# Performance work log

Hardware: AMD Instinct MI355X
Metric: run time of the kernel (lower is better)

## Reference

```python
import jax, jax.numpy as jnp
import numpy as np

# hyperparameters from init_kwargs
TEMP = 0.05
MOMENTUM = 0.2
ALPHA = 0.9
TEMP_DIST = 0.6
LAMBDA1 = 1.0
LAMBDA2 = 1.0
EPS_CONS = 2.0
NUM_SAMPLES = 8192
NUM_FEATURES = 2048
B = 256
K = 20
EPS = 1e-12


def setup_inputs() -> dict:
    key = jax.random.key(0)
    ks = jax.random.split(key, 8)
    inputs0 = jax.random.normal(ks[0], (B, NUM_FEATURES), dtype=jnp.float32)
    logits0 = jax.random.normal(ks[1], (B, NUM_SAMPLES), dtype=jnp.float32)
    logits1 = jax.random.normal(ks[2], (B, NUM_SAMPLES), dtype=jnp.float32)
    targets = jax.random.randint(ks[3], (B,), 0, NUM_SAMPLES, dtype=jnp.int32)
    indexes = jnp.arange(B, dtype=jnp.int32)  # global idx == batch idx (identity idx2bidx)
    neighbors = jax.random.randint(ks[4], (B, K), 0, B, dtype=jnp.int32)
    neighbor_dists = jax.random.uniform(ks[5], (B, K), dtype=jnp.float32)
    rampup = jnp.ones((), dtype=jnp.float32)
    features = jax.random.normal(ks[6], (NUM_SAMPLES, NUM_FEATURES), dtype=jnp.float32)
    features = features / jnp.linalg.norm(features, axis=1, keepdims=True)
    return {
        'inputs0': inputs0, 'logits0': logits0, 'logits1': logits1,
        'targets': targets, 'indexes': indexes, 'neighbors': neighbors,
        'neighbor_dists': neighbor_dists, 'rampup': rampup, 'features': features,
    }


def reference(inputs0, logits0, logits1, targets, indexes, neighbors,
              neighbor_dists, rampup, features):
    # F.normalize(inputs[0], dim=1)
    x = inputs0 / jnp.maximum(jnp.linalg.norm(inputs0, axis=1, keepdims=True), EPS)

    # CM forward: scores against memory bank, scaled by temperature
    outputs = (x @ features.T) / TEMP                      # [B, S]
    logp = jax.nn.log_softmax(outputs, axis=-1)
    loss_nce = -jnp.mean(jnp.take_along_axis(logp, targets[:, None], axis=1))

    targets_onehot = jax.nn.one_hot(targets, NUM_SAMPLES, dtype=logits0.dtype)

    # neighbor gathering: indexes = arange(B) so idx2bidx is identity; every
    # neighbor in [0,B) passes the `nb in indexes` filter.
    p0 = jax.nn.softmax(logits0, axis=-1)[neighbors]       # [B, K, S]
    p1 = jax.nn.softmax(logits1, axis=-1)[neighbors]       # [B, K, S]
    # loop appends logits0-row then logits1-row per neighbor -> interleave
    p = jnp.stack([p0, p1], axis=2).reshape(B, 2 * K, NUM_SAMPLES)
    d2 = jnp.repeat(neighbor_dists, 2, axis=1)             # [B, 2K] (d,d pairs)
    w = jax.nn.softmax(d2 / TEMP_DIST, axis=1)             # [B, 2K]
    logits_neighbors1 = jnp.einsum('bk,bks->bs', w, p)     # [B, S]

    # KL branch: neighbors with dist <= eps_consistency (all, since eps=2.0)
    mask = (neighbor_dists <= EPS_CONS).astype(p0.dtype)   # [B, K]
    cnt = jnp.maximum(mask.sum(axis=1, keepdims=True), 1.0)
    logits_neighbors1_KL = jnp.einsum('bk,bks->bs', mask, p0) / cnt  # [B, S]

    refined = ALPHA * targets_onehot + (1.0 - ALPHA) * jax.lax.stop_gradient(logits_neighbors1)
    loss_ce = jnp.mean(jnp.sum(-refined * jax.nn.log_softmax(logits0, axis=-1), axis=1))

    # KLDivLoss(logsoftmax(logits1).detach(), target) with batchmean reduction
    lp1 = jax.lax.stop_gradient(jax.nn.log_softmax(logits1, axis=-1))
    t = logits_neighbors1_KL
    kl = jnp.sum(jnp.where(t > 0, t * (jnp.log(jnp.maximum(t, EPS)) - lp1), 0.0)) / B

    # CM momentum memory-bank scatter update (backward side-effect in torch);
    # equivalent to the sequential loop when targets are unique in the batch.
    upd = MOMENTUM * features[targets] + (1.0 - MOMENTUM) * x
    upd = upd / jnp.maximum(jnp.linalg.norm(upd, axis=1, keepdims=True), EPS)
    new_features = features.at[targets].set(upd)

    return (loss_nce, LAMBDA1 * loss_ce, LAMBDA2 * rampup * kl, new_features)
```

## Files before the change

### kernel.cpp

```cpp
#include <hip/hip_runtime.h>
#include <cmath>

#define NB 256
#define NS 8192
#define NF 2048
#define NK 20

typedef _Float16 half8 __attribute__((ext_vector_type(8)));
typedef _Float16 half4 __attribute__((ext_vector_type(4)));
typedef float f32x4 __attribute__((ext_vector_type(4)));

__device__ __forceinline__ void async16(const void* g, void* l) {
  __builtin_amdgcn_global_load_lds(
      (const __attribute__((address_space(1))) unsigned int*)g,
      (__attribute__((address_space(3))) unsigned int*)l, 16, 0, 0);
}

__device__ __forceinline__ float waveSum(float v) {
#pragma unroll
  for (int off = 32; off > 0; off >>= 1) v += __shfl_xor(v, off, 64);
  return v;
}
__device__ __forceinline__ float waveMax(float v) {
#pragma unroll
  for (int off = 32; off > 0; off >>= 1) v = fmaxf(v, __shfl_xor(v, off, 64));
  return v;
}

__global__ __launch_bounds__(256, 1) void prep(
    const float* __restrict__ in0, const float* __restrict__ logits0,
    const float* __restrict__ logits1, const int* __restrict__ neighbors,
    const float* __restrict__ ndist, _Float16* __restrict__ Pt,
    _Float16* __restrict__ xh, _Float16* __restrict__ alpha_h,
    float* __restrict__ mll, _Float16* __restrict__ Wp,
    float* __restrict__ loss) {
  __shared__ alignas(16) union {
    struct {
      float redA[4];
      float redB[4];
    } s;
    _Float16 Lt[16 * 520];
  } sm;
  int tid = threadIdx.x, blk = blockIdx.x;
  int wave = tid >> 6, lane = tid & 63;

  if (blk < 512) {
    int r = blk;
    const float* src = (r < NB) ? logits0 : logits1;
    const float4* row = (const float4*)(src + (size_t)(r & (NB - 1)) * NS);
    float4 v[8];
    float mx = -1e30f;
#pragma unroll
    for (int i = 0; i < 8; ++i) {
      v[i] = row[tid + i * 256];
      mx = fmaxf(mx, fmaxf(fmaxf(v[i].x, v[i].y), fmaxf(v[i].z, v[i].w)));
    }
    float wv = waveMax(mx);
    if (lane == 0) sm.s.redA[wave] = wv;
    __syncthreads();
    float m = fmaxf(fmaxf(sm.s.redA[0], sm.s.redA[1]), fmaxf(sm.s.redA[2], sm.s.redA[3]));
    float se = 0.0f;
#pragma unroll
    for (int i = 0; i < 8; ++i)
      se += expf(v[i].x - m) + expf(v[i].y - m) + expf(v[i].z - m) + expf(v[i].w - m);
    float sw = waveSum(se);
    if (lane == 0) sm.s.redB[wave] = sw;
    __syncthreads();
    float l = (sm.s.redB[0] + sm.s.redB[1]) + (sm.s.redB[2] + sm.s.redB[3]);
    if (tid == 0) {
      mll[r] = m + logf(l);
      alpha_h[r] = (_Float16)(256.0f * expf(-m) / l);
    }
  } else if (blk < 1024) {
    int s0 = (blk - 512) * 16;
#pragma unroll
    for (int g = 0; g < 8; ++g) {
      int pos = g * 256 + tid;
      int row = pos >> 2, c4 = pos & 3;
      const float* src = ((row < NB) ? logits0 + (size_t)row * NS
                                     : logits1 + (size_t)(row - NB) * NS) + s0 + c4 * 4;
      float4 v = *(const float4*)src;
      sm.Lt[(c4 * 4 + 0) * 520 + row] = (_Float16)expf(v.x);
      sm.Lt[(c4 * 4 + 1) * 520 + row] = (_Float16)expf(v.y);
      sm.Lt[(c4 * 4 + 2) * 520 + row] = (_Float16)expf(v.z);
      sm.Lt[(c4 * 4 + 3) * 520 + row] = (_Float16)expf(v.w);
    }
    __syncthreads();
    int srow = tid >> 4, seg = tid & 15;
    _Float16* dst = Pt + (size_t)(s0 + srow) * 512 + seg * 32;
    const _Float16* lsrc = &sm.Lt[srow * 520 + seg * 32];
#pragma unroll
    for (int q = 0; q < 4; ++q)
      *(half8*)(dst + q * 8) = *(const half8*)(lsrc + q * 8);
  } else if (blk < 1280) {
    int b = blk - 1024;
    const float4* row = (const float4*)(in0 + (size_t)b * NF);
    float4 v0 = row[tid], v1 = row[tid + 256];
    float ss = v0.x * v0.x + v0.y * v0.y + v0.z * v0.z + v0.w * v0.w +
               v1.x * v1.x + v1.y * v1.y + v1.z * v1.z + v1.w * v1.w;
    float w = waveSum(ss);
    if (lane == 0) sm.s.redA[wave] = w;
    __syncthreads();
    float tot = (sm.s.redA[0] + sm.s.redA[1]) + (sm.s.redA[2] + sm.s.redA[3]);
    float inv = 1.0f / fmaxf(sqrtf(tot), 1e-12f);
    half4 h0, h1;
    h0[0] = (_Float16)(v0.x * inv); h0[1] = (_Float16)(v0.y * inv);
    h0[2] = (_Float16)(v0.z * inv); h0[3] = (_Float16)(v0.w * inv);
    h1[0] = (_Float16)(v1.x * inv); h1[1] = (_Float16)(v1.y * inv);
    h1[2] = (_Float16)(v1.z * inv); h1[3] = (_Float16)(v1.w * inv);
    ((half4*)(xh + (size_t)b * NF))[tid] = h0;
    ((half4*)(xh + (size_t)b * NF))[tid + 256] = h1;
  } else {
    if (tid < 3) loss[tid] = 0.0f;
    float4* W4 = (float4*)Wp;
    for (int i = tid; i < 512 * 512 * 2 / 16; i += 256) W4[i] = make_float4(0, 0, 0, 0);
    __syncthreads();
    int b = tid;
    float d[NK], e[NK];
    int n[NK];
    float s = 0.0f;
    int cnt = 0;
#pragma unroll
    for (int k = 0; k < NK; ++k) {
      d[k] = ndist[b * NK + k];
      n[k] = neighbors[b * NK + k];
      e[k] = expf(d[k] * (1.0f / 0.6f));
      s += e[k];
      cnt += (d[k] <= 2.0f) ? 1 : 0;
    }
    float invs = 1.0f / (2.0f * s);
    float invc = 1.0f / fmaxf((float)cnt, 1.0f);
    _Float16* rkl = Wp + (size_t)b * 512;
    _Float16* rce = Wp + (size_t)(256 + b) * 512;
#pragma unroll
    for (int k = 0; k < NK; ++k) {
      bool first = true;
#pragma unroll
      for (int k2 = 0; k2 < NK; ++k2)
        if (k2 < k && n[k2] == n[k]) first = false;
      if (first) {
        float wsum = 0.0f, ksum = 0.0f;
#pragma unroll
        for (int k2 = 0; k2 < NK; ++k2)
          if (k2 >= k && n[k2] == n[k]) {
            wsum += e[k2] * invs;
            ksum += (d[k2] <= 2.0f) ? invc : 0.0f;
          }
        rkl[n[k]] = (_Float16)ksum;
        rce[n[k]] = (_Float16)wsum;
        rce[256 + n[k]] = (_Float16)wsum;
      }
    }
  }
}

__global__ __launch_bounds__(256) void gemms(
    const _Float16* __restrict__ xh, const float* __restrict__ fB,
    const _Float16* __restrict__ Wp, const _Float16* __restrict__ Pt,
    const _Float16* __restrict__ alpha_h,
    const float* __restrict__ logits0, const float* __restrict__ logits1,
    const float* __restrict__ mll, const int* __restrict__ targets,
    float* __restrict__ outF, float* __restrict__ pm, float* __restrict__ pl,
    float* __restrict__ tgt, float* __restrict__ part) {
  __shared__ alignas(16) _Float16 As[128 * 64];
  __shared__ alignas(16) _Float16 Bs[128 * 64];
  __shared__ alignas(16) _Float16 Al[512];
  __shared__ float red[4];
  int tid = threadIdx.x, wave = tid >> 6, lane = tid & 63;
  int quad = lane >> 4, r16 = lane & 15, lrow = lane >> 3, lch = lane & 7;
  int blk = blockIdx.x;
  if (blk < 256) {
    int bx = blk & 127, by = blk >> 7;
    int n0 = bx * 64, m0 = by * 128;
    int c4 = tid & 15, rbase = tid >> 4;
    f32x4 acc[2][4] = {};
    for (int k0 = 0; k0 < NF; k0 += 64) {
      float4 bv[4];
#pragma unroll
      for (int ss = 0; ss < 4; ++ss)
        bv[ss] = *(const float4*)(fB + (size_t)(n0 + ss * 16 + rbase) * NF + k0 + c4 * 4);
      __syncthreads();
#pragma unroll
      for (int ss = 0; ss < 4; ++ss) {
        int rl = ss * 32 + wave * 8 + lrow;
        int sc = lch ^ (rl & 7);
        async16(xh + (size_t)(m0 + rl) * NF + k0 + sc * 8, &As[rl * 64 + lch * 8]);
      }
#pragma unroll
      for (int ss = 0; ss < 4; ++ss) {
        int row = ss * 16 + rbase;
        half4 h;
        h[0] = (_Float16)bv[ss].x; h[1] = (_Float16)bv[ss].y;
        h[2] = (_Float16)bv[ss].z; h[3] = (_Float16)bv[ss].w;
        int pc = (((c4 >> 1) ^ (row & 7)) << 3) + ((c4 & 1) << 2);
        *(half4*)&Bs[row * 64 + pc] = h;
        if (by == 0)
          *(float4*)(outF + (size_t)(n0 + row) * NF + k0 + c4 * 4) = bv[ss];
      }
      __syncthreads();
#pragma unroll
      for (int sub = 0; sub < 2; ++sub) {
        int slot = ((sub * 4 + quad) ^ (r16 & 7)) * 8;
        half8 af[2], bf[4];
#pragma unroll
        for (int i = 0; i < 2; ++i)
          af[i] = *(const half8*)&As[(wave * 32 + i * 16 + r16) * 64 + slot];
#pragma unroll
        for (int j = 0; j < 4; ++j)
          bf[j] = *(const half8*)&Bs[(j * 16 + r16) * 64 + slot];
#pragma unroll
        for (int i = 0; i < 2; ++i)
#pragma unroll
          for (int j = 0; j < 4; ++j)
            acc[i][j] = __builtin_amdgcn_mfma_f32_16x16x32_f16(af[i], bf[j], acc[i][j], 0, 0, 0);
      }
    }
#pragma unroll
    for (int i = 0; i < 2; ++i)
#pragma unroll
      for (int r = 0; r < 4; ++r) {
        int R = m0 + wave * 32 + i * 16 + quad * 4 + r;
        float sv[4];
#pragma unroll
        for (int j = 0; j < 4; ++j) sv[j] = acc[i][j][r] * 20.0f;
        float mx = fmaxf(fmaxf(sv[0], sv[1]), fmaxf(sv[2], sv[3]));
#pragma unroll
        for (int m2 = 1; m2 < 16; m2 <<= 1) mx = fmaxf(mx, __shfl_xor(mx, m2, 64));
        float e = expf(sv[0] - mx) + expf(sv[1] - mx) + expf(sv[2] - mx) + expf(sv[3] - mx);
#pragma unroll
        for (int m2 = 1; m2 < 16; m2 <<= 1) e += __shfl_xor(e, m2, 64);
        int tg = targets[R];
#pragma unroll
        for (int j = 0; j < 4; ++j)
          if (n0 + j * 16 + r16 == tg) tgt[R] = sv[j];
        if (r16 == 0) { pm[R * 128 + bx] = mx; pl[R * 128 + bx] = e; }
      }
  } else {
    int nb = blk - 256;
    int bx = nb & 63, by = nb >> 6;
    int n0 = bx * 128, m0 = by * 128;
    int wm = (wave >> 1) * 64, wn = (wave & 1) * 64;
    if (tid < 64) ((half8*)Al)[tid] = ((const half8*)alpha_h)[tid];
    f32x4 acc[4][4] = {};
    for (int k0 = 0; k0 < 512; k0 += 64) {
      __syncthreads();
#pragma unroll
      for (int ss = 0; ss < 4; ++ss) {
        int rl = ss * 32 + wave * 8 + lrow;
        int sc = lch ^ (rl & 7);
        async16(Wp + (size_t)(m0 + rl) * 512 + k0 + sc * 8, &As[rl * 64 + lch * 8]);
        async16(Pt + (size_t)(n0 + rl) * 512 + k0 + sc * 8, &Bs[rl * 64 + lch * 8]);
      }
      __syncthreads();
#pragma unroll
      for (int sub = 0; sub < 2; ++sub) {
        int slot = ((sub * 4 + quad) ^ (r16 & 7)) * 8;
        half8 alv = *(const half8*)&Al[k0 + slot];
        half8 af[4], bf[4];
#pragma unroll
        for (int i = 0; i < 4; ++i)
          af[i] = *(const half8*)&As[(wm + i * 16 + r16) * 64 + slot];
#pragma unroll
        for (int j = 0; j < 4; ++j)
          bf[j] = *(const half8*)&Bs[(wn + j * 16 + r16) * 64 + slot] * alv;
#pragma unroll
        for (int i = 0; i < 4; ++i)
#pragma unroll
          for (int j = 0; j < 4; ++j)
            acc[i][j] = __builtin_amdgcn_mfma_f32_16x16x32_f16(af[i], bf[j], acc[i][j], 0, 0, 0);
      }
    }
    bool iskl = (by < 2);
    const float* lgbase = iskl ? logits1 : logits0;
    float local = 0.0f;
#pragma unroll
    for (int i = 0; i < 4; ++i)
#pragma unroll
      for (int r = 0; r < 4; ++r) {
        int Mg = m0 + wm + i * 16 + quad * 4 + r;
        int b = iskl ? Mg : (Mg - 256);
        float mv = mll[iskl ? 256 + b : b];
        const float* lgrow = lgbase + (size_t)b * NS + n0 + wn;
#pragma unroll
        for (int j = 0; j < 4; ++j) {
          float lg = lgrow[j * 16 + r16];
          float t = acc[i][j][r] * (1.0f / 256.0f);
          if (iskl)
            local += (t > 0.0f) ? t * (logf(fmaxf(t, 1e-12f)) - (lg - mv)) : 0.0f;
          else
            local += -0.1f * t * (lg - mv);
        }
      }
    float wsv = waveSum(local);
    if (lane == 0) red[wave] = wsv;
    __syncthreads();
    if (tid == 0) part[nb] = (red[0] + red[1]) + (red[2] + red[3]);
  }
}

__global__ __launch_bounds__(128) void final_reduce(
    const float* __restrict__ pm, const float* __restrict__ pl,
    const float* __restrict__ tgt, const float* __restrict__ part,
    const float* __restrict__ logits0, const float* __restrict__ mll,
    const int* __restrict__ targets, const float* __restrict__ rampup,
    const float* __restrict__ in0, const float* __restrict__ features,
    float* __restrict__ outF, float* __restrict__ out) {
  __shared__ float rA[2], rB[2];
  __shared__ int flag;
  int tid = threadIdx.x, blk = blockIdx.x;
  if (blk < 256) {
    int b = blk;
    float m = pm[b * 128 + tid];
    float l = pl[b * 128 + tid];
    float wm = waveMax(m);
    if ((tid & 63) == 0) rA[tid >> 6] = wm;
    __syncthreads();
    float mx = fmaxf(rA[0], rA[1]);
    float e = l * expf(m - mx);
    float ws = waveSum(e);
    if ((tid & 63) == 0) rB[tid >> 6] = ws;
    __syncthreads();
    if (tid == 0) {
      float S = rB[0] + rB[1];
      float nce = -(tgt[b] - mx - logf(S));
      int tg = targets[b];
      float oh = -0.9f * (logits0[(size_t)b * NS + tg] - mll[b]);
      float pb = part[b];
      float v1 = oh;
      if (b >= 128) v1 += pb;
      atomicAdd(out + 0, nce * (1.0f / 256.0f));
      atomicAdd(out + 1, v1 * (1.0f / 256.0f));
      if (b < 128) atomicAdd(out + 2, rampup[0] * pb * (1.0f / 256.0f));
    }
  } else {
    int b = blk - 256;
    int tg = targets[b];
    if (tid == 0) flag = 0;
    __syncthreads();
    bool later = false;
    for (int i = b + 1 + tid; i < 256; i += 128) later = later || (targets[i] == tg);
    if (later) flag = 1;
    __syncthreads();
    if (flag) return;
    const float4* xr = (const float4*)(in0 + (size_t)b * NF);
    const float4* fr = (const float4*)(features + (size_t)tg * NF);
    float4 a[4];
    float ssx = 0.0f;
#pragma unroll
    for (int s = 0; s < 4; ++s) {
      a[s] = xr[tid + s * 128];
      ssx += a[s].x * a[s].x + a[s].y * a[s].y + a[s].z * a[s].z + a[s].w * a[s].w;
    }
    float w1 = waveSum(ssx);
    if ((tid & 63) == 0) rA[tid >> 6] = w1;
    __syncthreads();
    float ix = 0.8f / fmaxf(sqrtf(rA[0] + rA[1]), 1e-12f);
    float4 v[4];
    float ss = 0.0f;
#pragma unroll
    for (int s = 0; s < 4; ++s) {
      float4 f = fr[tid + s * 128];
      v[s] = make_float4(0.2f * f.x + ix * a[s].x, 0.2f * f.y + ix * a[s].y,
                         0.2f * f.z + ix * a[s].z, 0.2f * f.w + ix * a[s].w);
      ss += v[s].x * v[s].x + v[s].y * v[s].y + v[s].z * v[s].z + v[s].w * v[s].w;
    }
    float w2 = waveSum(ss);
    if ((tid & 63) == 0) rB[tid >> 6] = w2;
    __syncthreads();
    float inv = 1.0f / fmaxf(sqrtf(rB[0] + rB[1]), 1e-12f);
    float4* o4 = (float4*)(outF + (size_t)tg * NF);
#pragma unroll
    for (int s = 0; s < 4; ++s)
      o4[tid + s * 128] = make_float4(v[s].x * inv, v[s].y * inv, v[s].z * inv, v[s].w * inv);
  }
}

extern "C" void kernel_launch(void* const* d_in, const int* in_sizes, int n_in,
                              void* d_out, int out_size, void* d_ws, size_t ws_size,
                              hipStream_t stream) {
  const float* inputs0 = (const float*)d_in[0];
  const float* logits0 = (const float*)d_in[1];
  const float* logits1 = (const float*)d_in[2];
  const int* targets = (const int*)d_in[3];
  const int* neighbors = (const int*)d_in[5];
  const float* ndist = (const float*)d_in[6];
  const float* rampup = (const float*)d_in[7];
  const float* features = (const float*)d_in[8];
  float* out = (float*)d_out;

  char* ws = (char*)d_ws;
  float* mll = (float*)(ws + 4096);
  _Float16* alpha_h = (_Float16*)(ws + 8192);
  float* part = (float*)(ws + 12288);
  float* tgt = (float*)(ws + 16384);
  float* pm = (float*)(ws + 65536);
  float* pl = (float*)(ws + 196608);
  _Float16* Wp = (_Float16*)(ws + 524288);
  _Float16* xh = (_Float16*)(ws + (3 << 20));
  _Float16* Pt = (_Float16*)(ws + (4 << 20));

  prep<<<1281, 256, 0, stream>>>(inputs0, logits0, logits1, neighbors, ndist,
                                 Pt, xh, alpha_h, mll, Wp, out);
  gemms<<<512, 256, 0, stream>>>(xh, features, Wp, Pt, alpha_h, logits0, logits1,
                                 mll, targets, out + 3, pm, pl, tgt, part);
  final_reduce<<<512, 128, 0, stream>>>(pm, pl, tgt, part, logits0, mll, targets,
                                        rampup, inputs0, features, out + 3, out);
}
```

Before: 209.9 us.

## Parallelize neighbor-weight prep across blocks and deepen GEMM K-tile

The single prep block that zeroed the whole weight matrix and built every row's neighbor weights is split into 256 blocks. Each block zeroes its own two rows and builds them with one thread, which removes a long serial tail from the prep kernel. The first GEMM stage now uses a K-tile of 128 instead of 64, halving the number of loop iterations and barriers, at the cost of more LDS. The fp32 feature copy to the output is now split between the two row-tile blocks, half of the K range each, instead of being done only by the first block.

```diff
diff --git a/kernel.cpp b/kernel.cpp
--- a/kernel.cpp
+++ b/kernel.cpp
@@ -45,6 +45,7 @@
   int wave = tid >> 6, lane = tid & 63;
 
   if (blk < 512) {
+    if (blk == 0 && tid < 3) loss[tid] = 0.0f;
     int r = blk;
     const float* src = (r < NB) ? logits0 : logits1;
     const float4* row = (const float4*)(src + (size_t)(r & (NB - 1)) * NS);
@@ -111,44 +112,45 @@
     ((half4*)(xh + (size_t)b * NF))[tid] = h0;
     ((half4*)(xh + (size_t)b * NF))[tid + 256] = h1;
   } else {
-    if (tid < 3) loss[tid] = 0.0f;
-    float4* W4 = (float4*)Wp;
-    for (int i = tid; i < 512 * 512 * 2 / 16; i += 256) W4[i] = make_float4(0, 0, 0, 0);
-    __syncthreads();
-    int b = tid;
-    float d[NK], e[NK];
-    int n[NK];
-    float s = 0.0f;
-    int cnt = 0;
-#pragma unroll
-    for (int k = 0; k < NK; ++k) {
-      d[k] = ndist[b * NK + k];
-      n[k] = neighbors[b * NK + k];
-      e[k] = expf(d[k] * (1.0f / 0.6f));
-      s += e[k];
-      cnt += (d[k] <= 2.0f) ? 1 : 0;
-    }
-    float invs = 1.0f / (2.0f * s);
-    float invc = 1.0f / fmaxf((float)cnt, 1.0f);
+    int b = blk - 1280;
     _Float16* rkl = Wp + (size_t)b * 512;
     _Float16* rce = Wp + (size_t)(256 + b) * 512;
-#pragma unroll
-    for (int k = 0; k < NK; ++k) {
-      bool first = true;
-#pragma unroll
-      for (int k2 = 0; k2 < NK; ++k2)
-        if (k2 < k && n[k2] == n[k]) first = false;
-      if (first) {
-        float wsum = 0.0f, ksum = 0.0f;
+    if (tid < 64) ((float4*)rkl)[tid] = make_float4(0, 0, 0, 0);
+    else if (tid < 128) ((float4*)rce)[tid - 64] = make_float4(0, 0, 0, 0);
+    __syncthreads();
+    if (tid == 0) {
+      float d[NK], e[NK];
+      int n[NK];
+      float s = 0.0f;
+      int cnt = 0;
+#pragma unroll
+      for (int k = 0; k < NK; ++k) {
+        d[k] = ndist[b * NK + k];
+        n[k] = neighbors[b * NK + k];
+        e[k] = expf(d[k] * (1.0f / 0.6f));
+        s += e[k];
+        cnt += (d[k] <= 2.0f) ? 1 : 0;
+      }
+      float invs = 1.0f / (2.0f * s);
+      float invc = 1.0f / fmaxf((float)cnt, 1.0f);
+#pragma unroll
+      for (int k = 0; k < NK; ++k) {
+        bool first = true;
 #pragma unroll
         for (int k2 = 0; k2 < NK; ++k2)
-          if (k2 >= k && n[k2] == n[k]) {
-            wsum += e[k2] * invs;
-            ksum += (d[k2] <= 2.0f) ? invc : 0.0f;
-          }
-        rkl[n[k]] = (_Float16)ksum;
-        rce[n[k]] = (_Float16)wsum;
-        rce[256 + n[k]] = (_Float16)wsum;
+          if (k2 < k && n[k2] == n[k]) first = false;
+        if (first) {
+          float wsum = 0.0f, ksum = 0.0f;
+#pragma unroll
+          for (int k2 = 0; k2 < NK; ++k2)
+            if (k2 >= k && n[k2] == n[k]) {
+              wsum += e[k2] * invs;
+              ksum += (d[k2] <= 2.0f) ? invc : 0.0f;
+            }
+          rkl[n[k]] = (_Float16)ksum;
+          rce[n[k]] = (_Float16)wsum;
+          rce[256 + n[k]] = (_Float16)wsum;
+        }
       }
     }
   }
@@ -162,7 +164,7 @@
     const float* __restrict__ mll, const int* __restrict__ targets,
     float* __restrict__ outF, float* __restrict__ pm, float* __restrict__ pl,
     float* __restrict__ tgt, float* __restrict__ part) {
-  __shared__ alignas(16) _Float16 As[128 * 64];
+  __shared__ alignas(16) _Float16 As[128 * 128];
   __shared__ alignas(16) _Float16 Bs[128 * 64];
   __shared__ alignas(16) _Float16 Al[512];
   __shared__ float red[4];
@@ -172,42 +174,53 @@
   if (blk < 256) {
     int bx = blk & 127, by = blk >> 7;
     int n0 = bx * 64, m0 = by * 128;
-    int c4 = tid & 15, rbase = tid >> 4;
+    int rr = tid >> 4, cc = tid & 15;
     f32x4 acc[2][4] = {};
-    for (int k0 = 0; k0 < NF; k0 += 64) {
-      float4 bv[4];
-#pragma unroll
-      for (int ss = 0; ss < 4; ++ss)
-        bv[ss] = *(const float4*)(fB + (size_t)(n0 + ss * 16 + rbase) * NF + k0 + c4 * 4);
+    for (int k0 = 0; k0 < NF; k0 += 128) {
       __syncthreads();
+      float4 bv[4][2];
 #pragma unroll
       for (int ss = 0; ss < 4; ++ss) {
-        int rl = ss * 32 + wave * 8 + lrow;
-        int sc = lch ^ (rl & 7);
-        async16(xh + (size_t)(m0 + rl) * NF + k0 + sc * 8, &As[rl * 64 + lch * 8]);
-      }
+        int row = ss * 16 + rr;
+        int sc = cc ^ (row & 7);
+        const float* src = fB + (size_t)(n0 + row) * NF + k0 + sc * 8;
+        bv[ss][0] = *(const float4*)src;
+        bv[ss][1] = *(const float4*)(src + 4);
+      }
+#pragma unroll
+      for (int ss = 0; ss < 8; ++ss) {
+        int row = ss * 16 + rr;
+        int sc = cc ^ (row & 7);
+        async16(xh + (size_t)(m0 + row) * NF + k0 + sc * 8, &As[row * 128 + cc * 8]);
+      }
+      bool doStore = (by == ((k0 >= NF / 2) ? 1 : 0));
 #pragma unroll
       for (int ss = 0; ss < 4; ++ss) {
-        int row = ss * 16 + rbase;
-        half4 h;
-        h[0] = (_Float16)bv[ss].x; h[1] = (_Float16)bv[ss].y;
-        h[2] = (_Float16)bv[ss].z; h[3] = (_Float16)bv[ss].w;
-        int pc = (((c4 >> 1) ^ (row & 7)) << 3) + ((c4 & 1) << 2);
-        *(half4*)&Bs[row * 64 + pc] = h;
-        if (by == 0)
-          *(float4*)(outF + (size_t)(n0 + row) * NF + k0 + c4 * 4) = bv[ss];
+        int row = ss * 16 + rr;
+        int sc = cc ^ (row & 7);
+        half8 h;
+        h[0] = (_Float16)bv[ss][0].x; h[1] = (_Float16)bv[ss][0].y;
+        h[2] = (_Float16)bv[ss][0].z; h[3] = (_Float16)bv[ss][0].w;
+        h[4] = (_Float16)bv[ss][1].x; h[5] = (_Float16)bv[ss][1].y;
+        h[6] = (_Float16)bv[ss][1].z; h[7] = (_Float16)bv[ss][1].w;
+        *(half8*)&Bs[row * 128 + cc * 8] = h;
+        if (doStore) {
+          float4* o = (float4*)(outF + (size_t)(n0 + row) * NF + k0 + sc * 8);
+          o[0] = bv[ss][0];
+          o[1] = bv[ss][1];
+        }
       }
       __syncthreads();
 #pragma unroll
-      for (int sub = 0; sub < 2; ++sub) {
+      for (int sub = 0; sub < 4; ++sub) {
         int slot = ((sub * 4 + quad) ^ (r16 & 7)) * 8;
         half8 af[2], bf[4];
 #pragma unroll
         for (int i = 0; i < 2; ++i)
-          af[i] = *(const half8*)&As[(wave * 32 + i * 16 + r16) * 64 + slot];
+          af[i] = *(const half8*)&As[(wave * 32 + i * 16 + r16) * 128 + slot];
 #pragma unroll
         for (int j = 0; j < 4; ++j)
-          bf[j] = *(const half8*)&Bs[(j * 16 + r16) * 64 + slot];
+          bf[j] = *(const half8*)&Bs[(j * 16 + r16) * 128 + slot];
 #pragma unroll
         for (int i = 0; i < 2; ++i)
 #pragma unroll
@@ -399,7 +412,7 @@
   _Float16* xh = (_Float16*)(ws + (3 << 20));
   _Float16* Pt = (_Float16*)(ws + (4 << 20));
 
-  prep<<<1281, 256, 0, stream>>>(inputs0, logits0, logits1, neighbors, ndist,
+  prep<<<1536, 256, 0, stream>>>(inputs0, logits0, logits1, neighbors, ndist,
                                  Pt, xh, alpha_h, mll, Wp, out);
   gemms<<<512, 256, 0, stream>>>(xh, features, Wp, Pt, alpha_h, logits0, logits1,
                                  mll, targets, out + 3, pm, pl, tgt, part);
```

Result: faster. 195.7 us (-6.8%).

## Replace neighbor-weight GEMM with direct gather-accumulate and widen feature GEMM tiles

Applied to the files above, without the earlier changes.

Drops the dense weight-matrix GEMM that mixed neighbor probabilities through a transposed exp table. Each block now gathers the 20 neighbor rows of a row-major fp16 exp table directly and accumulates the CE and KL targets, writing the loss terms with atomics. This also removes the zeroing and building of the weight matrix. The feature GEMM now uses 256x64 tiles so each features column-block is read and copied once instead of twice. The cost is uncoalesced-ish gathered reads and a larger LDS footprint per block.

```diff
diff --git a/kernel.cpp b/kernel.cpp
--- a/kernel.cpp
+++ b/kernel.cpp
@@ -27,24 +27,17 @@
   return v;
 }
 
-__global__ __launch_bounds__(256, 1) void prep(
+__global__ __launch_bounds__(256) void prep(
     const float* __restrict__ in0, const float* __restrict__ logits0,
-    const float* __restrict__ logits1, const int* __restrict__ neighbors,
-    const float* __restrict__ ndist, _Float16* __restrict__ Pt,
-    _Float16* __restrict__ xh, _Float16* __restrict__ alpha_h,
-    float* __restrict__ mll, _Float16* __restrict__ Wp,
-    float* __restrict__ loss) {
-  __shared__ alignas(16) union {
-    struct {
-      float redA[4];
-      float redB[4];
-    } s;
-    _Float16 Lt[16 * 520];
-  } sm;
+    const float* __restrict__ logits1, _Float16* __restrict__ P,
+    _Float16* __restrict__ xh, float* __restrict__ alpha,
+    float* __restrict__ mll, float* __restrict__ loss) {
+  __shared__ float redA[4], redB[4];
   int tid = threadIdx.x, blk = blockIdx.x;
   int wave = tid >> 6, lane = tid & 63;
 
   if (blk < 512) {
+    if (blk == 0 && tid < 3) loss[tid] = 0.0f;
     int r = blk;
     const float* src = (r < NB) ? logits0 : logits1;
     const float4* row = (const float4*)(src + (size_t)(r & (NB - 1)) * NS);
@@ -56,52 +49,40 @@
       mx = fmaxf(mx, fmaxf(fmaxf(v[i].x, v[i].y), fmaxf(v[i].z, v[i].w)));
     }
     float wv = waveMax(mx);
-    if (lane == 0) sm.s.redA[wave] = wv;
-    __syncthreads();
-    float m = fmaxf(fmaxf(sm.s.redA[0], sm.s.redA[1]), fmaxf(sm.s.redA[2], sm.s.redA[3]));
+    if (lane == 0) redA[wave] = wv;
+    __syncthreads();
+    float m = fmaxf(fmaxf(redA[0], redA[1]), fmaxf(redA[2], redA[3]));
+    float em = expf(m);
     float se = 0.0f;
-#pragma unroll
-    for (int i = 0; i < 8; ++i)
-      se += expf(v[i].x - m) + expf(v[i].y - m) + expf(v[i].z - m) + expf(v[i].w - m);
+    half4* prow = (half4*)(P + (size_t)r * NS);
+#pragma unroll
+    for (int i = 0; i < 8; ++i) {
+      float e0 = expf(v[i].x - m), e1 = expf(v[i].y - m);
+      float e2 = expf(v[i].z - m), e3 = expf(v[i].w - m);
+      se += (e0 + e1) + (e2 + e3);
+      half4 h;
+      h[0] = (_Float16)(e0 * em); h[1] = (_Float16)(e1 * em);
+      h[2] = (_Float16)(e2 * em); h[3] = (_Float16)(e3 * em);
+      prow[tid + i * 256] = h;
+    }
     float sw = waveSum(se);
-    if (lane == 0) sm.s.redB[wave] = sw;
-    __syncthreads();
-    float l = (sm.s.redB[0] + sm.s.redB[1]) + (sm.s.redB[2] + sm.s.redB[3]);
+    if (lane == 0) redB[wave] = sw;
+    __syncthreads();
+    float l = (redB[0] + redB[1]) + (redB[2] + redB[3]);
     if (tid == 0) {
       mll[r] = m + logf(l);
-      alpha_h[r] = (_Float16)(256.0f * expf(-m) / l);
-    }
-  } else if (blk < 1024) {
-    int s0 = (blk - 512) * 16;
-#pragma unroll
-    for (int g = 0; g < 8; ++g) {
-      int pos = g * 256 + tid;
-      int row = pos >> 2, c4 = pos & 3;
-      const float* src = ((row < NB) ? logits0 + (size_t)row * NS
-                                     : logits1 + (size_t)(row - NB) * NS) + s0 + c4 * 4;
-      float4 v = *(const float4*)src;
-      sm.Lt[(c4 * 4 + 0) * 520 + row] = (_Float16)expf(v.x);
-      sm.Lt[(c4 * 4 + 1) * 520 + row] = (_Float16)expf(v.y);
-      sm.Lt[(c4 * 4 + 2) * 520 + row] = (_Float16)expf(v.z);
-      sm.Lt[(c4 * 4 + 3) * 520 + row] = (_Float16)expf(v.w);
-    }
-    __syncthreads();
-    int srow = tid >> 4, seg = tid & 15;
-    _Float16* dst = Pt + (size_t)(s0 + srow) * 512 + seg * 32;
-    const _Float16* lsrc = &sm.Lt[srow * 520 + seg * 32];
-#pragma unroll
-    for (int q = 0; q < 4; ++q)
-      *(half8*)(dst + q * 8) = *(const half8*)(lsrc + q * 8);
-  } else if (blk < 1280) {
-    int b = blk - 1024;
+      alpha[r] = 256.0f * expf(-m) / l;
+    }
+  } else {
+    int b = blk - 512;
     const float4* row = (const float4*)(in0 + (size_t)b * NF);
     float4 v0 = row[tid], v1 = row[tid + 256];
     float ss = v0.x * v0.x + v0.y * v0.y + v0.z * v0.z + v0.w * v0.w +
                v1.x * v1.x + v1.y * v1.y + v1.z * v1.z + v1.w * v1.w;
     float w = waveSum(ss);
-    if (lane == 0) sm.s.redA[wave] = w;
-    __syncthreads();
-    float tot = (sm.s.redA[0] + sm.s.redA[1]) + (sm.s.redA[2] + sm.s.redA[3]);
+    if (lane == 0) redA[wave] = w;
+    __syncthreads();
+    float tot = (redA[0] + redA[1]) + (redA[2] + redA[3]);
     float inv = 1.0f / fmaxf(sqrtf(tot), 1e-12f);
     half4 h0, h1;
     h0[0] = (_Float16)(v0.x * inv); h0[1] = (_Float16)(v0.y * inv);
@@ -110,199 +91,156 @@
     h1[2] = (_Float16)(v1.z * inv); h1[3] = (_Float16)(v1.w * inv);
     ((half4*)(xh + (size_t)b * NF))[tid] = h0;
     ((half4*)(xh + (size_t)b * NF))[tid + 256] = h1;
+  }
+}
+
+__global__ __launch_bounds__(256) void fused2(
+    const _Float16* __restrict__ xh, const float* __restrict__ fB,
+    const _Float16* __restrict__ P, const float* __restrict__ alpha,
+    const float* __restrict__ mll, const float* __restrict__ logits0,
+    const float* __restrict__ logits1, const int* __restrict__ targets,
+    const int* __restrict__ neighbors, const float* __restrict__ ndist,
+    const float* __restrict__ rampup, float* __restrict__ outF,
+    float* __restrict__ pm, float* __restrict__ pl, float* __restrict__ tgt,
+    float* __restrict__ out) {
+  __shared__ alignas(16) _Float16 As[256 * 64];
+  __shared__ alignas(16) _Float16 Bs[64 * 64];
+  __shared__ float red[8];
+  int tid = threadIdx.x, wave = tid >> 6, lane = tid & 63;
+  int quad = lane >> 4, r16 = lane & 15;
+  int blk = blockIdx.x;
+
+  if (blk < 128) {
+    int n0 = blk * 64;
+    int srow = tid >> 2, scg = tid & 3;
+    f32x4 acc[4][4] = {};
+    for (int k0 = 0; k0 < NF; k0 += 64) {
+      float4 fv[4];
+      const float* bsrc = fB + (size_t)(n0 + srow) * NF + k0 + scg * 16;
+#pragma unroll
+      for (int q = 0; q < 4; ++q) fv[q] = *(const float4*)(bsrc + q * 4);
+      __syncthreads();
+#pragma unroll
+      for (int ss = 0; ss < 8; ++ss) {
+        int rl = ss * 32 + (tid >> 3);
+        int sc = (tid & 7) ^ (rl & 7);
+        async16(xh + (size_t)rl * NF + k0 + sc * 8, &As[rl * 64 + (tid & 7) * 8]);
+      }
+#pragma unroll
+      for (int h = 0; h < 2; ++h) {
+        half8 hh;
+        hh[0] = (_Float16)fv[2 * h].x; hh[1] = (_Float16)fv[2 * h].y;
+        hh[2] = (_Float16)fv[2 * h].z; hh[3] = (_Float16)fv[2 * h].w;
+        hh[4] = (_Float16)fv[2 * h + 1].x; hh[5] = (_Float16)fv[2 * h + 1].y;
+        hh[6] = (_Float16)fv[2 * h + 1].z; hh[7] = (_Float16)fv[2 * h + 1].w;
+        int p = (scg * 2 + h) ^ (srow & 7);
+        *(half8*)&Bs[srow * 64 + p * 8] = hh;
+      }
+      float4* odst = (float4*)(outF + (size_t)(n0 + srow) * NF + k0 + scg * 16);
+#pragma unroll
+      for (int q = 0; q < 4; ++q) odst[q] = fv[q];
+      __syncthreads();
+#pragma unroll
+      for (int sub = 0; sub < 2; ++sub) {
+        int slot = ((sub * 4 + quad) ^ (r16 & 7)) * 8;
+        half8 af[4], bf[4];
+#pragma unroll
+        for (int i = 0; i < 4; ++i)
+          af[i] = *(const half8*)&As[(wave * 64 + i * 16 + r16) * 64 + slot];
+#pragma unroll
+        for (int j = 0; j < 4; ++j)
+          bf[j] = *(const half8*)&Bs[(j * 16 + r16) * 64 + slot];
+#pragma unroll
+        for (int i = 0; i < 4; ++i)
+#pragma unroll
+          for (int j = 0; j < 4; ++j)
+            acc[i][j] = __builtin_amdgcn_mfma_f32_16x16x32_f16(af[i], bf[j], acc[i][j], 0, 0, 0);
+      }
+    }
+#pragma unroll
+    for (int i = 0; i < 4; ++i)
+#pragma unroll
+      for (int r = 0; r < 4; ++r) {
+        int R = wave * 64 + i * 16 + quad * 4 + r;
+        float sv[4];
+#pragma unroll
+        for (int j = 0; j < 4; ++j) sv[j] = acc[i][j][r] * 20.0f;
+        float mx = fmaxf(fmaxf(sv[0], sv[1]), fmaxf(sv[2], sv[3]));
+#pragma unroll
+        for (int m2 = 1; m2 < 16; m2 <<= 1) mx = fmaxf(mx, __shfl_xor(mx, m2, 64));
+        float e = expf(sv[0] - mx) + expf(sv[1] - mx) + expf(sv[2] - mx) + expf(sv[3] - mx);
+#pragma unroll
+        for (int m2 = 1; m2 < 16; m2 <<= 1) e += __shfl_xor(e, m2, 64);
+        int tg = targets[R];
+#pragma unroll
+        for (int j = 0; j < 4; ++j)
+          if (n0 + j * 16 + r16 == tg) tgt[R] = sv[j];
+        if (r16 == 0) { pm[R * 128 + blk] = mx; pl[R * 128 + blk] = e; }
+      }
   } else {
-    if (tid < 3) loss[tid] = 0.0f;
-    float4* W4 = (float4*)Wp;
-    for (int i = tid; i < 512 * 512 * 2 / 16; i += 256) W4[i] = make_float4(0, 0, 0, 0);
-    __syncthreads();
-    int b = tid;
-    float d[NK], e[NK];
-    int n[NK];
+    int gb = blk - 128;
+    int b = gb >> 2, s0 = (gb & 3) * 2048;
     float s = 0.0f;
     int cnt = 0;
 #pragma unroll
     for (int k = 0; k < NK; ++k) {
-      d[k] = ndist[b * NK + k];
-      n[k] = neighbors[b * NK + k];
-      e[k] = expf(d[k] * (1.0f / 0.6f));
-      s += e[k];
-      cnt += (d[k] <= 2.0f) ? 1 : 0;
+      float d = ndist[b * NK + k];
+      s += expf(d * (1.0f / 0.6f));
+      cnt += (d <= 2.0f) ? 1 : 0;
     }
     float invs = 1.0f / (2.0f * s);
     float invc = 1.0f / fmaxf((float)cnt, 1.0f);
-    _Float16* rkl = Wp + (size_t)b * 512;
-    _Float16* rce = Wp + (size_t)(256 + b) * 512;
-#pragma unroll
+    float ce[8] = {0, 0, 0, 0, 0, 0, 0, 0};
+    float kl[8] = {0, 0, 0, 0, 0, 0, 0, 0};
+    int sc_ = s0 + tid * 8;
+#pragma unroll 4
     for (int k = 0; k < NK; ++k) {
-      bool first = true;
-#pragma unroll
-      for (int k2 = 0; k2 < NK; ++k2)
-        if (k2 < k && n[k2] == n[k]) first = false;
-      if (first) {
-        float wsum = 0.0f, ksum = 0.0f;
-#pragma unroll
-        for (int k2 = 0; k2 < NK; ++k2)
-          if (k2 >= k && n[k2] == n[k]) {
-            wsum += e[k2] * invs;
-            ksum += (d[k2] <= 2.0f) ? invc : 0.0f;
-          }
-        rkl[n[k]] = (_Float16)ksum;
-        rce[n[k]] = (_Float16)wsum;
-        rce[256 + n[k]] = (_Float16)wsum;
-      }
-    }
-  }
-}
-
-__global__ __launch_bounds__(256) void gemms(
-    const _Float16* __restrict__ xh, const float* __restrict__ fB,
-    const _Float16* __restrict__ Wp, const _Float16* __restrict__ Pt,
-    const _Float16* __restrict__ alpha_h,
-    const float* __restrict__ logits0, const float* __restrict__ logits1,
-    const float* __restrict__ mll, const int* __restrict__ targets,
-    float* __restrict__ outF, float* __restrict__ pm, float* __restrict__ pl,
-    float* __restrict__ tgt, float* __restrict__ part) {
-  __shared__ alignas(16) _Float16 As[128 * 64];
-  __shared__ alignas(16) _Float16 Bs[128 * 64];
-  __shared__ alignas(16) _Float16 Al[512];
-  __shared__ float red[4];
-  int tid = threadIdx.x, wave = tid >> 6, lane = tid & 63;
-  int quad = lane >> 4, r16 = lane & 15, lrow = lane >> 3, lch = lane & 7;
-  int blk = blockIdx.x;
-  if (blk < 256) {
-    int bx = blk & 127, by = blk >> 7;
-    int n0 = bx * 64, m0 = by * 128;
-    int c4 = tid & 15, rbase = tid >> 4;
-    f32x4 acc[2][4] = {};
-    for (int k0 = 0; k0 < NF; k0 += 64) {
-      float4 bv[4];
-#pragma unroll
-      for (int ss = 0; ss < 4; ++ss)
-        bv[ss] = *(const float4*)(fB + (size_t)(n0 + ss * 16 + rbase) * NF + k0 + c4 * 4);
-      __syncthreads();
-#pragma unroll
-      for (int ss = 0; ss < 4; ++ss) {
-        int rl = ss * 32 + wave * 8 + lrow;
-        int sc = lch ^ (rl & 7);
-        async16(xh + (size_t)(m0 + rl) * NF + k0 + sc * 8, &As[rl * 64 + lch * 8]);
-      }
-#pragma unroll
-      for (int ss = 0; ss < 4; ++ss) {
-        int row = ss * 16 + rbase;
-        half4 h;
-        h[0] = (_Float16)bv[ss].x; h[1] = (_Float16)bv[ss].y;
-        h[2] = (_Float16)bv[ss].z; h[3] = (_Float16)bv[ss].w;
-        int pc = (((c4 >> 1) ^ (row & 7)) << 3) + ((c4 & 1) << 2);
-        *(half4*)&Bs[row * 64 + pc] = h;
-        if (by == 0)
-          *(float4*)(outF + (size_t)(n0 + row) * NF + k0 + c4 * 4) = bv[ss];
-      }
-      __syncthreads();
-#pragma unroll
-      for (int sub = 0; sub < 2; ++sub) {
-        int slot = ((sub * 4 + quad) ^ (r16 & 7)) * 8;
-        half8 af[2], bf[4];
-#pragma unroll
-        for (int i = 0; i < 2; ++i)
-          af[i] = *(const half8*)&As[(wave * 32 + i * 16 + r16) * 64 + slot];
-#pragma unroll
-        for (int j = 0; j < 4; ++j)
-          bf[j] = *(const half8*)&Bs[(j * 16 + r16) * 64 + slot];
-#pragma unroll
-        for (int i = 0; i < 2; ++i)
-#pragma unroll
-          for (int j = 0; j < 4; ++j)
-            acc[i][j] = __builtin_amdgcn_mfma_f32_16x16x32_f16(af[i], bf[j], acc[i][j], 0, 0, 0);
-      }
-    }
-#pragma unroll
-    for (int i = 0; i < 2; ++i)
-#pragma unroll
-      for (int r = 0; r < 4; ++r) {
-        int R = m0 + wave * 32 + i * 16 + quad * 4 + r;
-        float sv[4];
-#pragma unroll
-        for (int j = 0; j < 4; ++j) sv[j] = acc[i][j][r] * 20.0f;
-        float mx = fmaxf(fmaxf(sv[0], sv[1]), fmaxf(sv[2], sv[3]));
-#pragma unroll
-        for (int m2 = 1; m2 < 16; m2 <<= 1) mx = fmaxf(mx, __shfl_xor(mx, m2, 64));
-        float e = expf(sv[0] - mx) + expf(sv[1] - mx) + expf(sv[2] - mx) + expf(sv[3] - mx);
-#pragma unroll
-        for (int m2 = 1; m2 < 16; m2 <<= 1) e += __shfl_xor(e, m2, 64);
-        int tg = targets[R];
-#pragma unroll
-        for (int j = 0; j < 4; ++j)
-          if (n0 + j * 16 + r16 == tg) tgt[R] = sv[j];
-        if (r16 == 0) { pm[R * 128 + bx] = mx; pl[R * 128 + bx] = e; }
-      }
-  } else {
-    int nb = blk - 256;
-    int bx = nb & 63, by = nb >> 6;
-    int n0 = bx * 128, m0 = by * 128;
-    int wm = (wave >> 1) * 64, wn = (wave & 1) * 64;
-    if (tid < 64) ((half8*)Al)[tid] = ((const half8*)alpha_h)[tid];
-    f32x4 acc[4][4] = {};
-    for (int k0 = 0; k0 < 512; k0 += 64) {
-      __syncthreads();
-#pragma unroll
-      for (int ss = 0; ss < 4; ++ss) {
-        int rl = ss * 32 + wave * 8 + lrow;
-        int sc = lch ^ (rl & 7);
-        async16(Wp + (size_t)(m0 + rl) * 512 + k0 + sc * 8, &As[rl * 64 + lch * 8]);
-        async16(Pt + (size_t)(n0 + rl) * 512 + k0 + sc * 8, &Bs[rl * 64 + lch * 8]);
-      }
-      __syncthreads();
-#pragma unroll
-      for (int sub = 0; sub < 2; ++sub) {
-        int slot = ((sub * 4 + quad) ^ (r16 & 7)) * 8;
-        half8 alv = *(const half8*)&Al[k0 + slot];
-        half8 af[4], bf[4];
-#pragma unroll
-        for (int i = 0; i < 4; ++i)
-          af[i] = *(const half8*)&As[(wm + i * 16 + r16) * 64 + slot];
-#pragma unroll
-        for (int j = 0; j < 4; ++j)
-          bf[j] = *(const half8*)&Bs[(wn + j * 16 + r16) * 64 + slot] * alv;
-#pragma unroll
-        for (int i = 0; i < 4; ++i)
-#pragma unroll
-          for (int j = 0; j < 4; ++j)
-            acc[i][j] = __builtin_amdgcn_mfma_f32_16x16x32_f16(af[i], bf[j], acc[i][j], 0, 0, 0);
-      }
-    }
-    bool iskl = (by < 2);
-    const float* lgbase = iskl ? logits1 : logits0;
-    float local = 0.0f;
-#pragma unroll
-    for (int i = 0; i < 4; ++i)
-#pragma unroll
-      for (int r = 0; r < 4; ++r) {
-        int Mg = m0 + wm + i * 16 + quad * 4 + r;
-        int b = iskl ? Mg : (Mg - 256);
-        float mv = mll[iskl ? 256 + b : b];
-        const float* lgrow = lgbase + (size_t)b * NS + n0 + wn;
-#pragma unroll
-        for (int j = 0; j < 4; ++j) {
-          float lg = lgrow[j * 16 + r16];
-          float t = acc[i][j][r] * (1.0f / 256.0f);
-          if (iskl)
-            local += (t > 0.0f) ? t * (logf(fmaxf(t, 1e-12f)) - (lg - mv)) : 0.0f;
-          else
-            local += -0.1f * t * (lg - mv);
-        }
-      }
-    float wsv = waveSum(local);
-    if (lane == 0) red[wave] = wsv;
-    __syncthreads();
-    if (tid == 0) part[nb] = (red[0] + red[1]) + (red[2] + red[3]);
+      float d = ndist[b * NK + k];
+      int n = neighbors[b * NK + k];
+      float wce = expf(d * (1.0f / 0.6f)) * invs;
+      float wkl = (d <= 2.0f) ? invc : 0.0f;
+      float a0 = alpha[n], a1 = alpha[256 + n];
+      float c0 = wce * a0, c1 = wce * a1, ck = wkl * a0;
+      half8 p0 = *(const half8*)(P + (size_t)n * NS + sc_);
+      half8 p1 = *(const half8*)(P + (size_t)(256 + n) * NS + sc_);
+#pragma unroll
+      for (int e2 = 0; e2 < 8; ++e2) {
+        float q0 = (float)p0[e2], q1 = (float)p1[e2];
+        ce[e2] += c0 * q0 + c1 * q1;
+        kl[e2] += ck * q0;
+      }
+    }
+    float mv0 = mll[b], mv1 = mll[256 + b];
+    const float* g0 = logits0 + (size_t)b * NS + sc_;
+    const float* g1 = logits1 + (size_t)b * NS + sc_;
+    float4 l0a = *(const float4*)g0, l0b = *(const float4*)(g0 + 4);
+    float4 l1a = *(const float4*)g1, l1b = *(const float4*)(g1 + 4);
+    float lg0[8] = {l0a.x, l0a.y, l0a.z, l0a.w, l0b.x, l0b.y, l0b.z, l0b.w};
+    float lg1[8] = {l1a.x, l1a.y, l1a.z, l1a.w, l1b.x, l1b.y, l1b.z, l1b.w};
+    float lce = 0.0f, lkl = 0.0f;
+#pragma unroll
+    for (int e2 = 0; e2 < 8; ++e2) {
+      float t = ce[e2] * (1.0f / 256.0f);
+      lce += t * (lg0[e2] - mv0);
+      float tk = kl[e2] * (1.0f / 256.0f);
+      lkl += (tk > 0.0f) ? tk * (logf(fmaxf(tk, 1e-12f)) - (lg1[e2] - mv1)) : 0.0f;
+    }
+    float wc = waveSum(lce), wk = waveSum(lkl);
+    if (lane == 0) { red[wave] = wc; red[4 + wave] = wk; }
+    __syncthreads();
+    if (tid == 0) {
+      float ce_t = (red[0] + red[1]) + (red[2] + red[3]);
+      float kl_t = (red[4] + red[5]) + (red[6] + red[7]);
+      atomicAdd(out + 1, -0.1f * ce_t * (1.0f / 256.0f));
+      atomicAdd(out + 2, rampup[0] * kl_t * (1.0f / 256.0f));
+    }
   }
 }
 
 __global__ __launch_bounds__(128) void final_reduce(
     const float* __restrict__ pm, const float* __restrict__ pl,
-    const float* __restrict__ tgt, const float* __restrict__ part,
-    const float* __restrict__ logits0, const float* __restrict__ mll,
-    const int* __restrict__ targets, const float* __restrict__ rampup,
+    const float* __restrict__ tgt, const float* __restrict__ logits0,
+    const float* __restrict__ mll, const int* __restrict__ targets,
     const float* __restrict__ in0, const float* __restrict__ features,
     float* __restrict__ outF, float* __restrict__ out) {
   __shared__ float rA[2], rB[2];
@@ -325,12 +263,8 @@
       float nce = -(tgt[b] - mx - logf(S));
       int tg = targets[b];
       float oh = -0.9f * (logits0[(size_t)b * NS + tg] - mll[b]);
-      float pb = part[b];
-      float v1 = oh;
-      if (b >= 128) v1 += pb;
       atomicAdd(out + 0, nce * (1.0f / 256.0f));
-      atomicAdd(out + 1, v1 * (1.0f / 256.0f));
-      if (b < 128) atomicAdd(out + 2, rampup[0] * pb * (1.0f / 256.0f));
+      atomicAdd(out + 1, oh * (1.0f / 256.0f));
     }
   } else {
     int b = blk - 256;
@@ -390,19 +324,17 @@
 
   char* ws = (char*)d_ws;
   float* mll = (float*)(ws + 4096);
-  _Float16* alpha_h = (_Float16*)(ws + 8192);
-  float* part = (float*)(ws + 12288);
+  float* alpha = (float*)(ws + 8192);
   float* tgt = (float*)(ws + 16384);
   float* pm = (float*)(ws + 65536);
   float* pl = (float*)(ws + 196608);
-  _Float16* Wp = (_Float16*)(ws + 524288);
   _Float16* xh = (_Float16*)(ws + (3 << 20));
-  _Float16* Pt = (_Float16*)(ws + (4 << 20));
-
-  prep<<<1281, 256, 0, stream>>>(inputs0, logits0, logits1, neighbors, ndist,
-                                 Pt, xh, alpha_h, mll, Wp, out);
-  gemms<<<512, 256, 0, stream>>>(xh, features, Wp, Pt, alpha_h, logits0, logits1,
-                                 mll, targets, out + 3, pm, pl, tgt, part);
-  final_reduce<<<512, 128, 0, stream>>>(pm, pl, tgt, part, logits0, mll, targets,
-                                        rampup, inputs0, features, out + 3, out);
-}
+  _Float16* P = (_Float16*)(ws + (4 << 20));
+
+  prep<<<768, 256, 0, stream>>>(inputs0, logits0, logits1, P, xh, alpha, mll, out);
+  fused2<<<1152, 256, 0, stream>>>(xh, features, P, alpha, mll, logits0, logits1,
+                                   targets, neighbors, ndist, rampup, out + 3,
+                                   pm, pl, tgt, out);
+  final_reduce<<<512, 128, 0, stream>>>(pm, pl, tgt, logits0, mll, targets,
+                                        inputs0, features, out + 3, out);
+}
```

Result: slower. 215.7 us (+2.8%).
